# Performance work log

Hardware: AMD Instinct MI355X
Metric: run time of the kernel (lower is better)

Reference implementation:

```python
import jax, jax.numpy as jnp
import numpy as np

# Enformer/Borzoi-style MHA with relative positional bias
B, T, C = 2, 1536, 1536          # batch, seq bins, input channels
H, K, V = 8, 64, 192             # heads, key_size, value_size
F = 32                           # num_position_features (borzoi, asymmetric: 2 * 16 basis)


def setup_inputs() -> dict:
    key = jax.random.key(0)
    ks = jax.random.split(key, 9)
    he = lambda fan_in: (2.0 / fan_in) ** 0.5  # he_normal scale
    return {
        "x": jax.random.normal(ks[0], (B, T, C), jnp.float32),
        "Wq": jax.random.normal(ks[1], (C, H * K), jnp.float32) * he(C),
        "Wk": jax.random.normal(ks[2], (C, H * K), jnp.float32) * he(C),
        "Wv": jax.random.normal(ks[3], (C, H * V), jnp.float32) * he(C),
        "Wr": jax.random.normal(ks[4], (F, H * K), jnp.float32) * he(F),
        "r_w_bias": jax.random.normal(ks[5], (1, H, 1, K), jnp.float32) * 0.02,
        "r_r_bias": jax.random.normal(ks[6], (1, H, 1, K), jnp.float32) * 0.02,
        "Wo": jax.random.normal(ks[7], (H * V, H * V), jnp.float32) * he(H * V),
        "bo": jnp.zeros((H * V,), jnp.float32),
    }


def positional_features(positions):
    """Borzoi central-mask basis, absolute=True, asymmetric -> [L, F]."""
    nb = F // 2
    pow_rate = np.exp(np.log(T + 1) / nb).astype(np.float32)
    center_widths = pow_rate ** jnp.arange(1, nb + 1, dtype=jnp.float32) - 1.0  # [nb]
    sign = jnp.sign(positions)
    abs_pos = jnp.abs(positions)
    emb = (center_widths[None, :] > abs_pos[:, None]).astype(jnp.float32)  # [L, nb]
    return jnp.concatenate([emb, sign[:, None] * emb], axis=-1)  # [L, 2*nb]


def relative_shift(x):
    """[B,H,T,2T-1] -> [B,H,T,T] relative-shift trick (pad, reshape, slice)."""
    b, h, t, l = x.shape
    x = jnp.pad(x, ((0, 0), (0, 0), (0, 0), (1, 0)))      # [b,h,t,l+1]
    x = x.reshape(b, h, l + 1, t)[:, :, 1:, :]             # [b,h,l,t]
    x = x.reshape(b, h, t, l)
    return x[..., :t]


def reference(x, Wq, Wk, Wv, Wr, r_w_bias, r_r_bias, Wo, bo):
    q = (x @ Wq).reshape(B, T, H, K).transpose(0, 2, 1, 3)   # [B,H,T,K]
    k = (x @ Wk).reshape(B, T, H, K).transpose(0, 2, 1, 3)
    v = (x @ Wv).reshape(B, T, H, V).transpose(0, 2, 1, 3)   # [B,H,T,V]
    q = q * (K ** -0.5)  # scaling=True

    distances = jnp.arange(-T + 1, T, dtype=jnp.float32)     # [2T-1]
    pe = positional_features(distances)                       # [2T-1, F]
    rk = (pe @ Wr).reshape(2 * T - 1, H, K)                   # [2T-1, H, K]

    content_logits = jnp.einsum('bhtk,bhsk->bhts', q + r_w_bias, k)   # [B,H,T,T]
    rel_logits = jnp.einsum('bhtk,rhk->bhtr', q + r_r_bias, rk)       # [B,H,T,2T-1]
    logits = content_logits + relative_shift(rel_logits)

    weights = jax.nn.softmax(logits, axis=-1)
    out = jnp.einsum('bhts,bhsv->bhtv', weights, v)          # [B,H,T,V]
    out = out.transpose(0, 2, 1, 3).reshape(B, T, H * V)     # [B,T,H*V]
    return out @ Wo + bo
```

## Files before the change

### kernel.cpp

```cpp
#include <hip/hip_runtime.h>
#include <hip/hip_bf16.h>

typedef __hip_bfloat16 bf16;
typedef unsigned short ushort;
typedef unsigned int uint;
typedef __attribute__((ext_vector_type(8))) short short8;
typedef __attribute__((ext_vector_type(4))) float f32x4;

#define Bsz 2
#define Tn  1536
#define Cn  1536
#define Hn  8
#define Kn  64
#define Vn  192

__device__ __forceinline__ ushort f2bs(float f) {
  union { bf16 h; ushort u; } cv;
  cv.h = __float2bfloat16(f);
  return cv.u;
}
__device__ __forceinline__ float bs2f(ushort u) {
  union { float f; uint v; } cv; cv.v = ((uint)u) << 16; return cv.f;
}

__device__ __forceinline__ void gld_lds16(const ushort* g, ushort* l) {
  __builtin_amdgcn_global_load_lds(
      (const __attribute__((address_space(1))) uint*)g,
      (__attribute__((address_space(3))) uint*)l, 16, 0, 0);
}

__global__ __launch_bounds__(256) void prep(
    const float* __restrict__ x,  const float* __restrict__ Wq,
    const float* __restrict__ Wk, const float* __restrict__ Wv,
    const float* __restrict__ Wo, const float* __restrict__ Wr,
    ushort* __restrict__ xb, ushort* __restrict__ Wt,
    ushort* __restrict__ Wot, ushort* __restrict__ rkdb,
    unsigned char* __restrict__ lutb) {
  const int z = blockIdx.z;
  if (z < 4) {
    if (z < 2 && blockIdx.x >= 16) return;
    const float* in = (z == 0) ? Wq : (z == 1) ? Wk : (z == 2) ? Wv : Wo;
    ushort* out = (z == 0) ? Wt : (z == 1) ? Wt + 512 * 1536
                : (z == 2) ? Wt + 1024 * 1536 : Wot;
    const int Cc = (z < 2) ? 512 : 1536;
    __shared__ float tile[32][33];
    const int bx = blockIdx.x * 32;
    const int by = blockIdx.y * 32;
    const int tx = threadIdx.x & 31, ty = threadIdx.x >> 5;
#pragma unroll
    for (int i = 0; i < 32; i += 8)
      tile[ty + i][tx] = in[(size_t)(by + ty + i) * Cc + bx + tx];
    __syncthreads();
#pragma unroll
    for (int i = 0; i < 32; i += 8)
      out[(size_t)(bx + ty + i) * 1536 + by + tx] = f2bs(tile[tx][ty + i]);
  } else if (z == 4) {
    const int n4 = 3072 * 1536 / 4;
    for (int i = (blockIdx.y * 48 + blockIdx.x) * 256 + threadIdx.x; i < n4;
         i += 2304 * 256) {
      float4 v = ((const float4*)x)[i];
      uint2 o;
      o.x = (uint)f2bs(v.x) | ((uint)f2bs(v.y) << 16);
      o.y = (uint)f2bs(v.z) | ((uint)f2bs(v.w) << 16);
      ((uint2*)xb)[i] = o;
    }
  } else {
    const int base = (blockIdx.y * 48 + blockIdx.x) * 256 + threadIdx.x;
    if (base < 8 * 40 * 64) {
      const int h = base / 2560, rem = base % 2560, u = rem >> 6, k = rem & 63;
      float acc = 0.f;
      if (u < 33) {
        const float sg = (u == 32) ? 0.f : (u < 16 ? 1.f : -1.f);
        const int c = (u == 32) ? 16 : (u < 16 ? u + 1 : u - 15);
#pragma unroll
        for (int i = 0; i < 16; i++)
          if (i >= 16 - c)
            acc += Wr[i * 512 + h * 64 + k] + sg * Wr[(16 + i) * 512 + h * 64 + k];
      }
      rkdb[h * 2560 + u * 64 + k] = f2bs(acc);
    } else if (base < 8 * 40 * 64 + 3072) {
      const int idx = base - 8 * 40 * 64;
      const int d = idx - 1535;
      const float ad = fabsf((float)d);
      int c = 0;
#pragma unroll
      for (int i = 0; i < 16; i++) {
        double cw = exp(log((double)(Tn + 1)) * (double)(i + 1) / 16.0) - 1.0;
        if ((float)cw > ad) c++;
      }
      lutb[idx] = (unsigned char)((d == 0) ? 32 : (d > 0 ? c - 1 : 15 + c));
    }
  }
}

__global__ __launch_bounds__(256) void gemm_qkv(
    const ushort* __restrict__ xb, const ushort* __restrict__ Wt,
    ushort* __restrict__ qb, ushort* __restrict__ kb, ushort* __restrict__ vtb) {
  __shared__ ushort Al[128 * 32];
  __shared__ ushort Bl[128 * 32];
  const int tid = threadIdx.x;
  const int w = tid >> 6, lane = tid & 63, quad = lane >> 4, ln = lane & 15;
  const int bm = blockIdx.y * 128, bn = blockIdx.x * 128;
  const int wm = (w & 1) * 64, wn = (w >> 1) * 64;
  f32x4 acc[4][4];
#pragma unroll
  for (int i = 0; i < 4; i++)
#pragma unroll
    for (int j = 0; j < 4; j++) acc[i][j] = (f32x4){0.f, 0.f, 0.f, 0.f};

  for (int k0 = 0; k0 < 1536; k0 += 32) {
    __syncthreads();
#pragma unroll
    for (int st = 0; st < 2; st++) {
      int idx = tid + st * 256;
      int row = idx >> 2, col = (idx & 3) * 8;
      gld_lds16(xb + (size_t)(bm + row) * 1536 + k0 + col, Al + idx * 8);
      gld_lds16(Wt + (size_t)(bn + row) * 1536 + k0 + col, Bl + idx * 8);
    }
    __syncthreads();
    short8 af[4], bfr[4];
#pragma unroll
    for (int t = 0; t < 4; t++) {
      af[t]  = *(const short8*)(Al + (wm + t * 16 + ln) * 32 + quad * 8);
      bfr[t] = *(const short8*)(Bl + (wn + t * 16 + ln) * 32 + quad * 8);
    }
#pragma unroll
    for (int mt = 0; mt < 4; mt++)
#pragma unroll
      for (int nt = 0; nt < 4; nt++)
        acc[mt][nt] = __builtin_amdgcn_mfma_f32_16x16x32_bf16(
            af[mt], bfr[nt], acc[mt][nt], 0, 0, 0);
  }

  if (bn < 512) {
#pragma unroll
    for (int mt = 0; mt < 4; mt++)
#pragma unroll
      for (int nt = 0; nt < 4; nt++)
#pragma unroll
        for (int r = 0; r < 4; r++) {
          int m = bm + wm + mt * 16 + quad * 4 + r;
          int n = bn + wn + nt * 16 + ln;
          qb[(size_t)m * 512 + n] = f2bs(acc[mt][nt][r] * 0.125f);
        }
  } else if (bn < 1024) {
#pragma unroll
    for (int mt = 0; mt < 4; mt++)
#pragma unroll
      for (int nt = 0; nt < 4; nt++)
#pragma unroll
        for (int r = 0; r < 4; r++) {
          int m = bm + wm + mt * 16 + quad * 4 + r;
          int n = bn - 512 + wn + nt * 16 + ln;
          kb[(size_t)m * 512 + n] = f2bs(acc[mt][nt][r]);
        }
  } else {
#pragma unroll
    for (int mt = 0; mt < 4; mt++)
#pragma unroll
      for (int nt = 0; nt < 4; nt++) {
        int vcol = bn - 1024 + wn + nt * 16 + ln;
        int m0 = bm + wm + mt * 16 + quad * 4;
        uint2 val;
        val.x = (uint)f2bs(acc[mt][nt][0]) | ((uint)f2bs(acc[mt][nt][1]) << 16);
        val.y = (uint)f2bs(acc[mt][nt][2]) | ((uint)f2bs(acc[mt][nt][3]) << 16);
        *(uint2*)(vtb + (size_t)vcol * 3072 + m0) = val;
      }
  }
}

__global__ __launch_bounds__(256) void dgemm(
    const ushort* __restrict__ qb, const float* __restrict__ rrb,
    const ushort* __restrict__ rkdb, ushort* __restrict__ Db) {
  const int t0 = blockIdx.x * 64, h = blockIdx.y, b = blockIdx.z;
  const int t = t0 + (threadIdx.x >> 2), uu = threadIdx.x & 3;
  const ushort* qrow = qb + (size_t)(b * Tn + t) * 512 + h * 64;
  float qf[64];
#pragma unroll
  for (int k8 = 0; k8 < 8; k8++) {
    short8 v = *(const short8*)(qrow + k8 * 8);
#pragma unroll
    for (int e = 0; e < 8; e++)
      qf[k8 * 8 + e] = bs2f(f2bs(bs2f((ushort)v[e]) + rrb[h * 64 + k8 * 8 + e]));
  }
#pragma unroll
  for (int j = 0; j < 9; j++) {
    int u = uu + 4 * j;
    if (u < 33) {
      float acc = 0.f;
#pragma unroll
      for (int k8 = 0; k8 < 8; k8++) {
        short8 rv = *(const short8*)(rkdb + h * 2560 + u * 64 + k8 * 8);
#pragma unroll
        for (int e = 0; e < 8; e++)
          acc += qf[k8 * 8 + e] * bs2f((ushort)rv[e]);
      }
      Db[((size_t)(b * 8 + h) * 1536 + t) * 40 + u] = f2bs(acc);
    }
  }
}

__global__ __launch_bounds__(256) void gemm_out(
    const ushort* __restrict__ att, const ushort* __restrict__ Wot,
    const float* __restrict__ bo, float* __restrict__ out) {
  __shared__ ushort Al[128 * 32];
  __shared__ ushort Bl[128 * 32];
  const int tid = threadIdx.x;
  const int w = tid >> 6, lane = tid & 63, quad = lane >> 4, ln = lane & 15;
  const int bm = blockIdx.y * 128, bn = blockIdx.x * 128;
  const int wm = (w & 1) * 64, wn = (w >> 1) * 64;
  f32x4 acc[4][4];
#pragma unroll
  for (int i = 0; i < 4; i++)
#pragma unroll
    for (int j = 0; j < 4; j++) acc[i][j] = (f32x4){0.f, 0.f, 0.f, 0.f};

  for (int k0 = 0; k0 < 1536; k0 += 32) {
    __syncthreads();
#pragma unroll
    for (int st = 0; st < 2; st++) {
      int idx = tid + st * 256;
      int row = idx >> 2, col = (idx & 3) * 8;
      gld_lds16(att + (size_t)(bm + row) * 1536 + k0 + col, Al + idx * 8);
      gld_lds16(Wot + (size_t)(bn + row) * 1536 + k0 + col, Bl + idx * 8);
    }
    __syncthreads();
    short8 af[4], bfr[4];
#pragma unroll
    for (int t = 0; t < 4; t++) {
      af[t]  = *(const short8*)(Al + (wm + t * 16 + ln) * 32 + quad * 8);
      bfr[t] = *(const short8*)(Bl + (wn + t * 16 + ln) * 32 + quad * 8);
    }
#pragma unroll
    for (int mt = 0; mt < 4; mt++)
#pragma unroll
      for (int nt = 0; nt < 4; nt++)
        acc[mt][nt] = __builtin_amdgcn_mfma_f32_16x16x32_bf16(
            af[mt], bfr[nt], acc[mt][nt], 0, 0, 0);
  }
#pragma unroll
  for (int mt = 0; mt < 4; mt++)
#pragma unroll
    for (int nt = 0; nt < 4; nt++)
#pragma unroll
      for (int r = 0; r < 4; r++) {
        int m = bm + wm + mt * 16 + quad * 4 + r;
        int n = bn + wn + nt * 16 + ln;
        out[(size_t)m * 1536 + n] = acc[mt][nt][r] + bo[n];
      }
}

__global__ __launch_bounds__(256, 3) void attn_mfma(
    const ushort* __restrict__ qb, const ushort* __restrict__ kb,
    const ushort* __restrict__ vtb, const ushort* __restrict__ Db,
    const unsigned char* __restrict__ lutb,
    const float* __restrict__ rwb,
    ushort* __restrict__ op0, ushort* __restrict__ op1,
    float2* __restrict__ mlb) {
  __shared__ __align__(16) char smem[50176];
  ushort* Kl = (ushort*)smem;
  ushort* Vl = (ushort*)(smem + 8192);
  ushort* Dl = (ushort*)(smem + 32768);
  unsigned char* Ll = (unsigned char*)(smem + 37888);

  const int L  = blockIdx.x + 24 * blockIdx.y + 192 * blockIdx.z;
  const int h  = L & 7;
  const int g  = L >> 3;
  const int bsk = g / 24;
  const int b  = bsk >> 1;
  const int sk = bsk & 1;
  const int t0 = (g - bsk * 24) * 64;
  const int bT = b * Tn;
  const int tid = threadIdx.x;
  const int w = tid >> 6, lane = tid & 63, quad = lane >> 4, ln = lane & 15;

  ushort* Pp = (ushort*)(smem + 40960 + w * 2304);

  const int lr  = lane >> 3;
  const int lcx = (lane & 7) ^ lr;

  {
    const int s0 = sk * 768;
#pragma unroll
    for (int i = 0; i < 2; i++) {
      int kc = w * 2 + i, sr = kc * 8 + lr;
      gld_lds16(kb + (size_t)(bT + s0 + sr) * 512 + h * 64 + lcx * 8,
                (ushort*)(smem + kc * 1024) + lane * 8);
    }
#pragma unroll
    for (int i = 0; i < 6; i++) {
      int kc = w * 6 + i, vr = kc * 8 + lr;
      gld_lds16(vtb + (size_t)(h * 192 + vr) * 3072 + bT + s0 + lcx * 8,
                (ushort*)(smem + 8192 + kc * 1024) + lane * 8);
    }
    const ushort* dsrc = Db + ((size_t)(b * 8 + h) * 1536 + t0) * 40;
    gld_lds16(dsrc + w * 512 + lane * 8,
              (ushort*)(smem + 32768 + w * 1024) + lane * 8);
    if (w == 0)
      gld_lds16(dsrc + 4 * 512 + lane * 8,
                (ushort*)(smem + 32768 + 4096) + lane * 8);
    if (w < 3)
      gld_lds16((const ushort*)(lutb + w * 1024) + lane * 8,
                (ushort*)(smem + 37888 + w * 1024) + lane * 8);
  }

  short8 qw8[2];
  {
    const ushort* qrow = qb + (size_t)(bT + t0 + 16 * w + ln) * 512 + h * 64;
#pragma unroll
    for (int ks = 0; ks < 2; ks++) {
      int k0 = quad * 8 + ks * 32;
#pragma unroll
      for (int e = 0; e < 8; e++)
        qw8[ks][e] = (short)f2bs(bs2f(qrow[k0 + e]) + rwb[h * 64 + k0 + e]);
    }
  }

  f32x4 Oacc[12];
  float m_i[4], l_i[4];
#pragma unroll
  for (int vt = 0; vt < 12; vt++) Oacc[vt] = (f32x4){0.f, 0.f, 0.f, 0.f};
#pragma unroll
  for (int r = 0; r < 4; r++) { m_i[r] = -1e30f; l_i[r] = 0.f; }

  __syncthreads();

  const int ibase = sk * 768 - t0 - 16 * w - 4 * quad + ln + 1535;
  const int tl0 = 16 * w + 4 * quad;

  for (int ch = 0; ch < 12; ch++) {
    const int s0 = sk * 768 + ch * 64;

    f32x4 Sacc[4];
    __builtin_amdgcn_s_setprio(1);
#pragma unroll
    for (int ct = 0; ct < 4; ct++) {
      Sacc[ct] = (f32x4){0.f, 0.f, 0.f, 0.f};
#pragma unroll
      for (int ks = 0; ks < 2; ks++) {
        short8 bfr = *(const short8*)(
            Kl + (16 * ct + ln) * 64 + ((quad + 4 * ks) ^ (ln & 7)) * 8);
        Sacc[ct] = __builtin_amdgcn_mfma_f32_16x16x32_bf16(qw8[ks], bfr, Sacc[ct], 0, 0, 0);
      }
    }
    __builtin_amdgcn_s_setprio(0);

    float pS[4][4];
#pragma unroll
    for (int ct = 0; ct < 4; ct++)
#pragma unroll
      for (int r = 0; r < 4; r++) {
        int idx = ibase + 64 * ch + 16 * ct - r;
        int u = Ll[idx];
        pS[ct][r] = Sacc[ct][r] + bs2f(Dl[(tl0 + r) * 40 + u]);
      }

    __syncthreads();

    if (ch < 11) {
      const int s0n = s0 + 64;
#pragma unroll
      for (int i = 0; i < 2; i++) {
        int kc = w * 2 + i, sr = kc * 8 + lr;
        gld_lds16(kb + (size_t)(bT + s0n + sr) * 512 + h * 64 + lcx * 8,
                  (ushort*)(smem + kc * 1024) + lane * 8);
      }
    }

    float alpha[4];
#pragma unroll
    for (int r = 0; r < 4; r++) {
      float mx = fmaxf(fmaxf(pS[0][r], pS[1][r]), fmaxf(pS[2][r], pS[3][r]));
#pragma unroll
      for (int off = 8; off >= 1; off >>= 1) mx = fmaxf(mx, __shfl_xor(mx, off));
      float mnew = fmaxf(m_i[r], mx);
      alpha[r] = __expf(m_i[r] - mnew);
      m_i[r] = mnew;
      float rs = 0.f;
#pragma unroll
      for (int ct = 0; ct < 4; ct++) {
        pS[ct][r] = __expf(pS[ct][r] - mnew);
        rs += pS[ct][r];
      }
#pragma unroll
      for (int off = 8; off >= 1; off >>= 1) rs += __shfl_xor(rs, off);
      l_i[r] = l_i[r] * alpha[r] + rs;
    }
#pragma unroll
    for (int vt = 0; vt < 12; vt++)
#pragma unroll
      for (int r = 0; r < 4; r++) Oacc[vt][r] *= alpha[r];
#pragma unroll
    for (int ct = 0; ct < 4; ct++)
#pragma unroll
      for (int r = 0; r < 4; r++)
        Pp[(4 * quad + r) * 72 + 16 * ct + ln] = f2bs(pS[ct][r]);
    __asm__ volatile("s_waitcnt lgkmcnt(0)" ::: "memory");

    short8 afr[2];
#pragma unroll
    for (int ks = 0; ks < 2; ks++)
      afr[ks] = *(const short8*)(Pp + ln * 72 + quad * 8 + ks * 32);
    __builtin_amdgcn_s_setprio(1);
#pragma unroll
    for (int vt = 0; vt < 12; vt++) {
#pragma unroll
      for (int ks = 0; ks < 2; ks++) {
        short8 bfr = *(const short8*)(
            Vl + (16 * vt + ln) * 64 + ((quad + 4 * ks) ^ (ln & 7)) * 8);
        Oacc[vt] = __builtin_amdgcn_mfma_f32_16x16x32_bf16(afr[ks], bfr, Oacc[vt], 0, 0, 0);
      }
    }
    __builtin_amdgcn_s_setprio(0);

    __syncthreads();

    if (ch < 11) {
      const int s0n = s0 + 64;
#pragma unroll
      for (int i = 0; i < 6; i++) {
        int kc = w * 6 + i, vr = kc * 8 + lr;
        gld_lds16(vtb + (size_t)(h * 192 + vr) * 3072 + bT + s0n + lcx * 8,
                  (ushort*)(smem + 8192 + kc * 1024) + lane * 8);
      }
    }
  }

  ushort* op = sk ? op1 : op0;
  float inv[4];
#pragma unroll
  for (int r = 0; r < 4; r++) inv[r] = 1.f / l_i[r];
#pragma unroll
  for (int vt = 0; vt < 12; vt++)
#pragma unroll
    for (int r = 0; r < 4; r++) {
      int t = t0 + 16 * w + 4 * quad + r;
      op[(size_t)(bT + t) * 1536 + h * 192 + 16 * vt + ln] = f2bs(Oacc[vt][r] * inv[r]);
    }
  if (ln == 0) {
#pragma unroll
    for (int r = 0; r < 4; r++) {
      int t = t0 + 16 * w + 4 * quad + r;
      float2 v; v.x = m_i[r]; v.y = l_i[r];
      mlb[((sk * 2 + b) * 8 + h) * 1536 + t] = v;
    }
  }
}

__global__ __launch_bounds__(256) void attn_combine(
    const ushort* __restrict__ op0, const ushort* __restrict__ op1,
    const float2* __restrict__ mlb, ushort* __restrict__ att) {
  int g = blockIdx.x * 256 + threadIdx.x;
  int row = g / 384;
  int c4 = (g - row * 384) * 4;
  int b = row >= 1536;
  int t = row - b * 1536;
  int h = c4 / 192;
  float2 ml0 = mlb[((0 + b) * 8 + h) * 1536 + t];
  float2 ml1 = mlb[((2 + b) * 8 + h) * 1536 + t];
  float M = fmaxf(ml0.x, ml1.x);
  float w0 = __expf(ml0.x - M) * ml0.y;
  float w1 = __expf(ml1.x - M) * ml1.y;
  float inv = 1.f / (w0 + w1);
  w0 *= inv; w1 *= inv;
  size_t off = (size_t)row * 1536 + c4;
  uint2 a = *(const uint2*)(op0 + off);
  uint2 c = *(const uint2*)(op1 + off);
  uint2 o;
  float r0 = w0 * bs2f((ushort)(a.x & 0xffff)) + w1 * bs2f((ushort)(c.x & 0xffff));
  float r1 = w0 * bs2f((ushort)(a.x >> 16))    + w1 * bs2f((ushort)(c.x >> 16));
  float r2 = w0 * bs2f((ushort)(a.y & 0xffff)) + w1 * bs2f((ushort)(c.y & 0xffff));
  float r3 = w0 * bs2f((ushort)(a.y >> 16))    + w1 * bs2f((ushort)(c.y >> 16));
  o.x = (uint)f2bs(r0) | ((uint)f2bs(r1) << 16);
  o.y = (uint)f2bs(r2) | ((uint)f2bs(r3) << 16);
  *(uint2*)(att + off) = o;
}

extern "C" void kernel_launch(void* const* d_in, const int* in_sizes, int n_in,
                              void* d_out, int out_size, void* d_ws, size_t ws_size,
                              hipStream_t stream) {
  const float* x   = (const float*)d_in[0];
  const float* Wq  = (const float*)d_in[1];
  const float* Wk  = (const float*)d_in[2];
  const float* Wv  = (const float*)d_in[3];
  const float* Wr  = (const float*)d_in[4];
  const float* rwb = (const float*)d_in[5];
  const float* rrb = (const float*)d_in[6];
  const float* Wo  = (const float*)d_in[7];
  const float* bo  = (const float*)d_in[8];
  float* out = (float*)d_out;

  char* ws = (char*)d_ws;
  ushort* xb  = (ushort*)ws;
  ushort* op1 = (ushort*)ws;
  ushort* att = (ushort*)ws;
  ushort* Wot = (ushort*)(ws + 9437184);
  ushort* Wt  = (ushort*)(ws + 14155776);
  ushort* op0 = (ushort*)(ws + 14155776);
  ushort* qb  = (ushort*)(ws + 23592960);
  ushort* kb  = (ushort*)(ws + 26738688);
  ushort* vtb = (ushort*)(ws + 29884416);
  ushort* Db   = (ushort*)(ws + 39321600);
  unsigned char* lutb = (unsigned char*)(ws + 41287680);
  ushort* rkdb = (ushort*)(ws + 41290752);
  float2* mlb = (float2*)(ws + 42467328);

  prep<<<dim3(48, 48, 6), dim3(256), 0, stream>>>(
      x, Wq, Wk, Wv, Wo, Wr, xb, Wt, Wot, rkdb, lutb);
  gemm_qkv<<<dim3(20, 24), dim3(256), 0, stream>>>(xb, Wt, qb, kb, vtb);
  dgemm<<<dim3(24, 8, 2), dim3(256), 0, stream>>>(qb, rrb, rkdb, Db);
  attn_mfma<<<dim3(24, 8, 4), dim3(256), 0, stream>>>(
      qb, kb, vtb, Db, lutb, rwb, op0, op1, mlb);
  attn_combine<<<dim3(4608), dim3(256), 0, stream>>>(op0, op1, mlb, att);
  gemm_out<<<dim3(12, 24), dim3(256), 0, stream>>>(att, Wot, bo, out);
}
```

Baseline: 254.2 us.

## Fuse relative-position D GEMM into attention kernel via MFMA and move K prefetch sync

Removes the separate dgemm kernel and computes the 33-column relative bias table per query tile inside attn_mfma using MFMA on q+r_r_bias against rkdb, writing it straight to shared memory. This drops a launch and the global round trip of the D buffer. The loop is also reordered: bias gathers are hoisted before the QK MFMAs, and the barrier plus next-K prefetch moves after the P fragment reads. The cost is some redundant D computation per split-key block (each of the two sk halves computes it) and slightly different scheduling within the loop.

```diff
diff --git a/kernel.cpp b/kernel.cpp
--- a/kernel.cpp
+++ b/kernel.cpp
@@ -169,37 +169,6 @@
   }
 }
 
-__global__ __launch_bounds__(256) void dgemm(
-    const ushort* __restrict__ qb, const float* __restrict__ rrb,
-    const ushort* __restrict__ rkdb, ushort* __restrict__ Db) {
-  const int t0 = blockIdx.x * 64, h = blockIdx.y, b = blockIdx.z;
-  const int t = t0 + (threadIdx.x >> 2), uu = threadIdx.x & 3;
-  const ushort* qrow = qb + (size_t)(b * Tn + t) * 512 + h * 64;
-  float qf[64];
-#pragma unroll
-  for (int k8 = 0; k8 < 8; k8++) {
-    short8 v = *(const short8*)(qrow + k8 * 8);
-#pragma unroll
-    for (int e = 0; e < 8; e++)
-      qf[k8 * 8 + e] = bs2f(f2bs(bs2f((ushort)v[e]) + rrb[h * 64 + k8 * 8 + e]));
-  }
-#pragma unroll
-  for (int j = 0; j < 9; j++) {
-    int u = uu + 4 * j;
-    if (u < 33) {
-      float acc = 0.f;
-#pragma unroll
-      for (int k8 = 0; k8 < 8; k8++) {
-        short8 rv = *(const short8*)(rkdb + h * 2560 + u * 64 + k8 * 8);
-#pragma unroll
-        for (int e = 0; e < 8; e++)
-          acc += qf[k8 * 8 + e] * bs2f((ushort)rv[e]);
-      }
-      Db[((size_t)(b * 8 + h) * 1536 + t) * 40 + u] = f2bs(acc);
-    }
-  }
-}
-
 __global__ __launch_bounds__(256) void gemm_out(
     const ushort* __restrict__ att, const ushort* __restrict__ Wot,
     const float* __restrict__ bo, float* __restrict__ out) {
@@ -252,9 +221,9 @@
 
 __global__ __launch_bounds__(256, 3) void attn_mfma(
     const ushort* __restrict__ qb, const ushort* __restrict__ kb,
-    const ushort* __restrict__ vtb, const ushort* __restrict__ Db,
+    const ushort* __restrict__ vtb, const ushort* __restrict__ rkdb,
     const unsigned char* __restrict__ lutb,
-    const float* __restrict__ rwb,
+    const float* __restrict__ rwb, const float* __restrict__ rrb,
     ushort* __restrict__ op0, ushort* __restrict__ op1,
     float2* __restrict__ mlb) {
   __shared__ __align__(16) char smem[50176];
@@ -293,26 +262,48 @@
       gld_lds16(vtb + (size_t)(h * 192 + vr) * 3072 + bT + s0 + lcx * 8,
                 (ushort*)(smem + 8192 + kc * 1024) + lane * 8);
     }
-    const ushort* dsrc = Db + ((size_t)(b * 8 + h) * 1536 + t0) * 40;
-    gld_lds16(dsrc + w * 512 + lane * 8,
-              (ushort*)(smem + 32768 + w * 1024) + lane * 8);
-    if (w == 0)
-      gld_lds16(dsrc + 4 * 512 + lane * 8,
-                (ushort*)(smem + 32768 + 4096) + lane * 8);
     if (w < 3)
       gld_lds16((const ushort*)(lutb + w * 1024) + lane * 8,
                 (ushort*)(smem + 37888 + w * 1024) + lane * 8);
   }
 
-  short8 qw8[2];
+  short8 qw8[2], qr8[2];
   {
     const ushort* qrow = qb + (size_t)(bT + t0 + 16 * w + ln) * 512 + h * 64;
 #pragma unroll
     for (int ks = 0; ks < 2; ks++) {
       int k0 = quad * 8 + ks * 32;
 #pragma unroll
-      for (int e = 0; e < 8; e++)
-        qw8[ks][e] = (short)f2bs(bs2f(qrow[k0 + e]) + rwb[h * 64 + k0 + e]);
+      for (int e = 0; e < 8; e++) {
+        float qv = bs2f(qrow[k0 + e]);
+        qw8[ks][e] = (short)f2bs(qv + rwb[h * 64 + k0 + e]);
+        qr8[ks][e] = (short)f2bs(qv + rrb[h * 64 + k0 + e]);
+      }
+    }
+  }
+
+  {
+    f32x4 Dacc[3];
+#pragma unroll
+    for (int ut = 0; ut < 3; ut++) {
+      Dacc[ut] = (f32x4){0.f, 0.f, 0.f, 0.f};
+#pragma unroll
+      for (int ks = 0; ks < 2; ks++) {
+        int urow = 16 * ut + ln; urow = urow > 39 ? 39 : urow;
+        short8 bfr = *(const short8*)(rkdb + h * 2560 + urow * 64 + quad * 8 + ks * 32);
+        Dacc[ut] = __builtin_amdgcn_mfma_f32_16x16x32_bf16(qr8[ks], bfr, Dacc[ut], 0, 0, 0);
+      }
+    }
+    const int trow = 16 * w + 4 * quad;
+#pragma unroll
+    for (int ut = 0; ut < 2; ut++)
+#pragma unroll
+      for (int r = 0; r < 4; r++)
+        Dl[(trow + r) * 40 + 16 * ut + ln] = f2bs(Dacc[ut][r]);
+    if (ln == 0) {
+#pragma unroll
+      for (int r = 0; r < 4; r++)
+        Dl[(trow + r) * 40 + 32] = f2bs(Dacc[2][r]);
     }
   }
 
@@ -329,7 +320,14 @@
   const int tl0 = 16 * w + 4 * quad;
 
   for (int ch = 0; ch < 12; ch++) {
-    const int s0 = sk * 768 + ch * 64;
+    float dval[4][4];
+#pragma unroll
+    for (int ct = 0; ct < 4; ct++)
+#pragma unroll
+      for (int r = 0; r < 4; r++) {
+        int idx = ibase + 64 * ch + 16 * ct - r;
+        dval[ct][r] = bs2f(Dl[(tl0 + r) * 40 + Ll[idx]]);
+      }
 
     f32x4 Sacc[4];
     __builtin_amdgcn_s_setprio(1);
@@ -349,23 +347,8 @@
 #pragma unroll
     for (int ct = 0; ct < 4; ct++)
 #pragma unroll
-      for (int r = 0; r < 4; r++) {
-        int idx = ibase + 64 * ch + 16 * ct - r;
-        int u = Ll[idx];
-        pS[ct][r] = Sacc[ct][r] + bs2f(Dl[(tl0 + r) * 40 + u]);
-      }
-
-    __syncthreads();
-
-    if (ch < 11) {
-      const int s0n = s0 + 64;
-#pragma unroll
-      for (int i = 0; i < 2; i++) {
-        int kc = w * 2 + i, sr = kc * 8 + lr;
-        gld_lds16(kb + (size_t)(bT + s0n + sr) * 512 + h * 64 + lcx * 8,
-                  (ushort*)(smem + kc * 1024) + lane * 8);
-      }
-    }
+      for (int r = 0; r < 4; r++)
+        pS[ct][r] = Sacc[ct][r] + dval[ct][r];
 
     float alpha[4];
 #pragma unroll
@@ -396,11 +379,23 @@
       for (int r = 0; r < 4; r++)
         Pp[(4 * quad + r) * 72 + 16 * ct + ln] = f2bs(pS[ct][r]);
     __asm__ volatile("s_waitcnt lgkmcnt(0)" ::: "memory");
-
     short8 afr[2];
 #pragma unroll
     for (int ks = 0; ks < 2; ks++)
       afr[ks] = *(const short8*)(Pp + ln * 72 + quad * 8 + ks * 32);
+
+    __syncthreads();
+
+    if (ch < 11) {
+      const int s0n = sk * 768 + ch * 64 + 64;
+#pragma unroll
+      for (int i = 0; i < 2; i++) {
+        int kc = w * 2 + i, sr = kc * 8 + lr;
+        gld_lds16(kb + (size_t)(bT + s0n + sr) * 512 + h * 64 + lcx * 8,
+                  (ushort*)(smem + kc * 1024) + lane * 8);
+      }
+    }
+
     __builtin_amdgcn_s_setprio(1);
 #pragma unroll
     for (int vt = 0; vt < 12; vt++) {
@@ -416,7 +411,7 @@
     __syncthreads();
 
     if (ch < 11) {
-      const int s0n = s0 + 64;
+      const int s0n = sk * 768 + ch * 64 + 64;
 #pragma unroll
       for (int i = 0; i < 6; i++) {
         int kc = w * 6 + i, vr = kc * 8 + lr;
@@ -500,7 +495,6 @@
   ushort* qb  = (ushort*)(ws + 23592960);
   ushort* kb  = (ushort*)(ws + 26738688);
   ushort* vtb = (ushort*)(ws + 29884416);
-  ushort* Db   = (ushort*)(ws + 39321600);
   unsigned char* lutb = (unsigned char*)(ws + 41287680);
   ushort* rkdb = (ushort*)(ws + 41290752);
   float2* mlb = (float2*)(ws + 42467328);
@@ -508,9 +502,8 @@
   prep<<<dim3(48, 48, 6), dim3(256), 0, stream>>>(
       x, Wq, Wk, Wv, Wo, Wr, xb, Wt, Wot, rkdb, lutb);
   gemm_qkv<<<dim3(20, 24), dim3(256), 0, stream>>>(xb, Wt, qb, kb, vtb);
-  dgemm<<<dim3(24, 8, 2), dim3(256), 0, stream>>>(qb, rrb, rkdb, Db);
   attn_mfma<<<dim3(24, 8, 4), dim3(256), 0, stream>>>(
-      qb, kb, vtb, Db, lutb, rwb, op0, op1, mlb);
+      qb, kb, vtb, rkdb, lutb, rwb, rrb, op0, op1, mlb);
   attn_combine<<<dim3(4608), dim3(256), 0, stream>>>(op0, op1, mlb, att);
   gemm_out<<<dim3(12, 24), dim3(256), 0, stream>>>(att, Wot, bo, out);
 }
```

New measurement: 236.2 us. 7.1% less time.
